# Optimization experiments

Measured on AMD Instinct MI355X. Metric: run time of the kernel, lower is better.

The kernel has to match this reference:

```python
import jax, jax.numpy as jnp
import numpy as np

H = 2048        # hidden_size
NH = 32         # num_heads
HD = H // NH    # head_dim = 64
S = 512         # seq_len
UP = 2          # upsample_ratio
SU = S * UP     # upsampled seq len = 1024
INTER = 5632    # GatedMLP intermediate: int(2048*4*2/3) rounded up to mult of 256
EPS = 1e-6
DEPTH = 1


def rmsnorm(x, w):
    var = jnp.mean(jnp.square(x), axis=-1, keepdims=True)
    return x * jax.lax.rsqrt(var + EPS) * w


def setup_inputs() -> dict:
    key = jax.random.key(0)
    ks = jax.random.split(key, 12)
    sc = 0.02
    return {
        "hidden_states": jax.random.normal(ks[0], (2, S, H), dtype=jnp.float32),
        "W_up": jax.random.normal(ks[1], (SU, S), dtype=jnp.float32) * sc,
        "b_up": jnp.zeros((SU,), dtype=jnp.float32),
        "attn_norm_w": jnp.ones((H,), dtype=jnp.float32),
        "Wq": jax.random.normal(ks[2], (H, H), dtype=jnp.float32) * sc,
        "Wk": jax.random.normal(ks[3], (H, H), dtype=jnp.float32) * sc,
        "Wv": jax.random.normal(ks[4], (H, H), dtype=jnp.float32) * sc,
        "Wo": jax.random.normal(ks[5], (H, H), dtype=jnp.float32) * sc,
        "mlp_norm_w": jnp.ones((H,), dtype=jnp.float32),
        "Wg": jax.random.normal(ks[6], (INTER, H), dtype=jnp.float32) * sc,
        "Wu": jax.random.normal(ks[7], (INTER, H), dtype=jnp.float32) * sc,
        "Wd": jax.random.normal(ks[8], (H, INTER), dtype=jnp.float32) * sc,
    }


def reference(hidden_states, W_up, b_up, attn_norm_w, Wq, Wk, Wv, Wo,
              mlp_norm_w, Wg, Wu, Wd):
    B = hidden_states.shape[0]
    # init_upsampled_tokens: Linear over the sequence axis
    # up[b,t,d] = sum_s h[b,s,d] * W_up[t,s] + b_up[t]
    up = jnp.einsum('bsd,ts->btd', hidden_states, W_up) + b_up[None, :, None]

    for _ in range(DEPTH):
        residual = jnp.concatenate([hidden_states, up], axis=-2)  # [B, S+SU, H]
        x = rmsnorm(up, attn_norm_w)                               # [B, SU, H]
        q = (x @ Wq.T).reshape(B, SU, NH, HD)
        k = (residual @ Wk.T).reshape(B, S + SU, NH, HD)
        v = (residual @ Wv.T).reshape(B, S + SU, NH, HD)
        # explicit (non-causal) cross-attention, full score matrix
        scores = jnp.einsum('bshd,bthd->bsht', q, k) / np.sqrt(HD).astype(np.float32)
        attn = jax.nn.softmax(scores, axis=-1)
        o = jnp.einsum('bsht,bthd->bshd', attn, v).reshape(B, SU, H)
        x = (o @ Wo.T) + x                 # residual onto the *normed* tokens
        x = rmsnorm(x, mlp_norm_w)
        mlp_out = (jax.nn.silu(x @ Wg.T) * (x @ Wu.T)) @ Wd.T
        up = mlp_out + x
    return up
```

## Files before the change

kernel.cpp:

```cpp
#include <hip/hip_runtime.h>

typedef __bf16 bf16;
typedef __bf16 bf16x8 __attribute__((ext_vector_type(8)));
typedef float  f32x4  __attribute__((ext_vector_type(4)));
typedef unsigned int u32x4 __attribute__((ext_vector_type(4)));

#define NB 2
#define SS 512
#define HH 2048
#define SUx 1024
#define TT 1536
#define INTERx 5632

__device__ __forceinline__ void gload16(const void* g, void* l)
{
    __builtin_amdgcn_global_load_lds(
        (const __attribute__((address_space(1))) void*)g,
        (__attribute__((address_space(3))) void*)l, 16, 0, 0);
}

__global__ __launch_bounds__(256)
void cast_k(const float* __restrict__ in, bf16* __restrict__ out, long n)
{
    long i = ((long)blockIdx.x * 256 + threadIdx.x) * 8;
    if (i >= n) return;
    f32x4 a = *(const f32x4*)(in + i);
    f32x4 b = *(const f32x4*)(in + i + 4);
    bf16x8 o;
    o[0]=(bf16)a[0]; o[1]=(bf16)a[1]; o[2]=(bf16)a[2]; o[3]=(bf16)a[3];
    o[4]=(bf16)b[0]; o[5]=(bf16)b[1]; o[6]=(bf16)b[2]; o[7]=(bf16)b[3];
    *(bf16x8*)(out + i) = o;
}

template <typename TIN>
__global__ __launch_bounds__(256)
void transpose_k(const TIN* __restrict__ in, bf16* __restrict__ out,
                 int inRS, int outRS, int nz2,
                 long inZ1, long inZ2, long outZ1, long outZ2)
{
    __shared__ bf16 tile[64][65];
    int z1 = blockIdx.z / nz2, z2 = blockIdx.z % nz2;
    const TIN* ip = in + (long)z1*inZ1 + (long)z2*inZ2
                  + (long)blockIdx.x*64*inRS + (long)blockIdx.y*64;
    bf16* op = out + (long)z1*outZ1 + (long)z2*outZ2
             + (long)blockIdx.y*64*outRS + (long)blockIdx.x*64;
    int tc = threadIdx.x & 63, tr = threadIdx.x >> 6;
    #pragma unroll
    for (int rr = 0; rr < 64; rr += 4)
        tile[rr+tr][tc] = (bf16)(float)ip[(long)(rr+tr)*inRS + tc];
    __syncthreads();
    #pragma unroll
    for (int cc = 0; cc < 64; cc += 4)
        op[(long)(cc+tr)*outRS + tc] = tile[tc][cc+tr];
}

__global__ __launch_bounds__(256)
void rmsnorm_k(const float* __restrict__ x, const float* __restrict__ w,
               bf16* __restrict__ yb, float* __restrict__ yf)
{
    long row = blockIdx.x;
    const float* xp = x + row * HH;
    int t = threadIdx.x;
    f32x4 v0 = *(const f32x4*)(xp + t*8);
    f32x4 v1 = *(const f32x4*)(xp + t*8 + 4);
    float ss = 0.f;
    #pragma unroll
    for (int j = 0; j < 4; ++j) ss += v0[j]*v0[j] + v1[j]*v1[j];
    #pragma unroll
    for (int off = 32; off > 0; off >>= 1) ss += __shfl_xor(ss, off);
    __shared__ float red[4];
    if ((t & 63) == 0) red[t >> 6] = ss;
    __syncthreads();
    float tot = red[0] + red[1] + red[2] + red[3];
    float inv = rsqrtf(tot * (1.0f/(float)HH) + 1e-6f);
    f32x4 w0 = *(const f32x4*)(w + t*8);
    f32x4 w1 = *(const f32x4*)(w + t*8 + 4);
    f32x4 y0, y1; bf16x8 ob;
    #pragma unroll
    for (int j = 0; j < 4; ++j) {
        y0[j] = v0[j] * inv * w0[j];
        y1[j] = v1[j] * inv * w1[j];
        ob[j]   = (bf16)y0[j];
        ob[4+j] = (bf16)y1[j];
    }
    *(bf16x8*)(yb + row*HH + t*8) = ob;
    if (yf) {
        *(f32x4*)(yf + row*HH + t*8)     = y0;
        *(f32x4*)(yf + row*HH + t*8 + 4) = y1;
    }
}

template <int GU>
__global__ __launch_bounds__(512)
void gemm_k(const bf16* __restrict__ A, const bf16* __restrict__ Bw,
            int Nsplit, int K,
            long sA, long sB,
            bf16* __restrict__ Cb, bf16* __restrict__ Cb2, long sCb,
            float* __restrict__ C32, long sC32,
            const float* __restrict__ res, long sRes,
            const float* __restrict__ bias,
            float scale, int doSilu)
{
    __shared__ alignas(16) bf16 As[2][128 * 64];
    __shared__ alignas(16) bf16 Bs[2][128 * 64];
    int z = blockIdx.z;
    const bf16* Ap = A + (long)z * sA;

    int gx = gridDim.x;
    int nwg = gx * gridDim.y;
    int lin = blockIdx.y * gx + blockIdx.x;
    int qq = nwg >> 3, r8 = nwg & 7;
    int xcd = lin & 7, off = lin >> 3;
    int wg = (xcd < r8 ? xcd * (qq + 1) : r8 * (qq + 1) + (xcd - r8) * qq) + off;
    int n0 = (wg % gx) * 128, m0 = (wg / gx) * 128;

    int t = threadIdx.x, lane = t & 63, w = t >> 6;
    int wr = w >> 2, wc = w & 3;
    int lc = lane & 15, lg = lane >> 4;

    int lr = lane >> 3, ls = lane & 7;
    const bf16* gA[2]; const bf16* gB[2];
    int ldsOff[2];
    #pragma unroll
    for (int i = 0; i < 2; ++i) {
        int r = (i*8 + w)*8 + lr;
        gA[i] = Ap + (long)(m0 + r) * K + (ls ^ lr) * 8;
        if (GU) {
            long grow = (long)(n0 >> 1) + (r >> 1);
            gB[i] = Bw + ((r & 1) ? (long)INTERx * K : 0) + grow * K + (ls ^ lr) * 8;
        } else {
            const bf16* Bp = Bw + (long)z * sB;
            gB[i] = Bp + (long)(n0 + r) * K + (ls ^ lr) * 8;
        }
        ldsOff[i] = (i*8 + w) * 512;
    }

    f32x4 zero = {0.f, 0.f, 0.f, 0.f};
    f32x4 acc[4][2];
    #pragma unroll
    for (int i = 0; i < 4; ++i)
        #pragma unroll
        for (int j = 0; j < 2; ++j) acc[i][j] = zero;

    int NKI = K >> 6;
    #pragma unroll
    for (int i = 0; i < 2; ++i) {
        gload16(gA[i], &As[0][0] + ldsOff[i]);
        gload16(gB[i], &Bs[0][0] + ldsOff[i]);
    }
    if (NKI > 1) {
        #pragma unroll
        for (int i = 0; i < 2; ++i) {
            gload16(gA[i] + 64, &As[1][0] + ldsOff[i]);
            gload16(gB[i] + 64, &Bs[1][0] + ldsOff[i]);
        }
    }

    for (int ks = 0; ks < NKI; ++ks) {
        int cur = ks & 1;
        const bf16* Asc = &As[cur][0];
        const bf16* Bsc = &Bs[cur][0];

        if (ks == NKI - 1) asm volatile("s_waitcnt vmcnt(0)" ::: "memory");
        else               asm volatile("s_waitcnt vmcnt(4)" ::: "memory");
        __builtin_amdgcn_s_barrier();
        __builtin_amdgcn_sched_barrier(0);

        #pragma unroll
        for (int kk = 0; kk < 2; ++kk) {
            bf16x8 af[4], bfv[2];
            #pragma unroll
            for (int i = 0; i < 4; ++i) {
                int rA = wr*64 + i*16 + lc;
                af[i]  = *(const bf16x8*)(Asc + rA*64 + (((kk*4 + lg) ^ (rA & 7)) * 8));
            }
            #pragma unroll
            for (int j = 0; j < 2; ++j) {
                int rB = wc*32 + j*16 + lc;
                bfv[j] = *(const bf16x8*)(Bsc + rB*64 + (((kk*4 + lg) ^ (rB & 7)) * 8));
            }
            __builtin_amdgcn_s_setprio(1);
            #pragma unroll
            for (int i = 0; i < 4; ++i)
                #pragma unroll
                for (int j = 0; j < 2; ++j)
                    acc[i][j] = __builtin_amdgcn_mfma_f32_16x16x32_bf16(af[i], bfv[j], acc[i][j], 0, 0, 0);
            __builtin_amdgcn_s_setprio(0);
        }

        __builtin_amdgcn_s_barrier();
        if (ks + 2 < NKI) {
            long ko = (long)(ks + 2) * 64;
            #pragma unroll
            for (int i = 0; i < 2; ++i) {
                gload16(gA[i] + ko, (bf16*)Asc + ldsOff[i]);
                gload16(gB[i] + ko, (bf16*)Bsc + ldsOff[i]);
            }
        }
    }

    if (GU) {
        #pragma unroll
        for (int i = 0; i < 4; ++i) {
            #pragma unroll
            for (int j = 0; j < 2; ++j) {
                int tc2 = wc*32 + j*16 + lc;
                int colp = (n0 >> 1) + (tc2 >> 1);
                #pragma unroll
                for (int r = 0; r < 4; ++r) {
                    int row = m0 + wr*64 + i*16 + lg*4 + r;
                    float v = acc[i][j][r];
                    float pv = __shfl_xor(v, 1);
                    float g  = (lc & 1) ? pv : v;
                    float uu = (lc & 1) ? v  : pv;
                    float prod = (g / (1.f + __expf(-g))) * uu;
                    if (!(lc & 1))
                        Cb[(long)row * Nsplit + colp] = (bf16)prod;
                }
            }
        }
    } else {
        #pragma unroll
        for (int i = 0; i < 4; ++i) {
            #pragma unroll
            for (int j = 0; j < 2; ++j) {
                int col = n0 + wc*32 + j*16 + lc;
                bf16* dst = Cb; int c2 = col;
                if (Cb2 && col >= Nsplit) { dst = Cb2; c2 = col - Nsplit; }
                int firstHalf = (col < Nsplit);
                #pragma unroll
                for (int r = 0; r < 4; ++r) {
                    int row = m0 + wr*64 + i*16 + lg*4 + r;
                    float v = acc[i][j][r] * scale;
                    if (bias)   v += bias[row];
                    if (doSilu && firstHalf) v = v / (1.f + __expf(-v));
                    long off = (long)row * Nsplit + c2;
                    if (res)  v += res[(long)z * sRes + off];
                    if (C32)  C32[(long)z * sC32 + off] = v;
                    if (dst)  dst[(long)z * sCb + off] = (bf16)v;
                }
            }
        }
    }
}

__global__ __launch_bounds__(512)
void attn_k(const bf16* __restrict__ q, const bf16* __restrict__ k,
            const bf16* __restrict__ vt, bf16* __restrict__ o)
{
    int qc = blockIdx.x, h = blockIdx.y, b = blockIdx.z;
    int t = threadIdx.x, lane = t & 63, w = t >> 6;
    int lc = lane & 15, lg = lane >> 4;
    const bf16* qp = q  + ((long)(b*SUx + qc*256 + w*32)) * HH + h*64;
    const bf16* kp = k  + ((long)b*TT) * HH + h*64;
    const bf16* vp = vt + ((long)(b*32 + h)) * 64 * TT;

    __shared__ alignas(16) bf16 Ks[2][64*64];
    __shared__ alignas(16) bf16 Vs[2][64*64];
    __shared__ alignas(16) bf16 Ps[8][2][16*72];

    bf16x8 qf[2][2];
    #pragma unroll
    for (int s = 0; s < 2; ++s)
        #pragma unroll
        for (int kk = 0; kk < 2; ++kk)
            qf[s][kk] = *(const bf16x8*)(qp + (long)(s*16 + lc)*HH + kk*32 + lg*8);

    int lr = lane >> 3, ls = lane & 7;
    int srow = w*8 + lr;
    int sslot = ls ^ lr;
    const bf16* gK = kp + (long)srow * HH + sslot*8;
    const bf16* gV = vp + (long)srow * TT + sslot*8;
    int ldsO = w * 512;

    f32x4 zero = {0.f, 0.f, 0.f, 0.f};
    f32x4 oacc[2][4];
    float lsum[2][4];
    #pragma unroll
    for (int qs = 0; qs < 2; ++qs) {
        #pragma unroll
        for (int r = 0; r < 4; ++r) lsum[qs][r] = 0.f;
        #pragma unroll
        for (int dt = 0; dt < 4; ++dt) oacc[qs][dt] = zero;
    }

    const int NS = TT / 64;
    gload16(gK,            &Ks[0][0] + ldsO);
    gload16(gV,            &Vs[0][0] + ldsO);
    gload16(gK + 64L*HH,   &Ks[1][0] + ldsO);
    gload16(gV + 64,       &Vs[1][0] + ldsO);

    for (int st = 0; st < NS; ++st) {
        int cur = st & 1;
        const bf16* Kc = &Ks[cur][0];
        const bf16* Vc = &Vs[cur][0];

        if (st == NS - 1) asm volatile("s_waitcnt vmcnt(0)" ::: "memory");
        else              asm volatile("s_waitcnt vmcnt(2)" ::: "memory");
        __builtin_amdgcn_s_barrier();
        __builtin_amdgcn_sched_barrier(0);

        bf16x8 kf[4][2];
        #pragma unroll
        for (int s2 = 0; s2 < 4; ++s2) {
            int row = s2*16 + lc;
            #pragma unroll
            for (int kk = 0; kk < 2; ++kk)
                kf[s2][kk] = *(const bf16x8*)(Kc + row*64 + (((kk*4 + lg) ^ (row & 7)) * 8));
        }
        f32x4 sv[2][4];
        __builtin_amdgcn_s_setprio(1);
        #pragma unroll
        for (int qs = 0; qs < 2; ++qs)
            #pragma unroll
            for (int s2 = 0; s2 < 4; ++s2) {
                f32x4 a0 = __builtin_amdgcn_mfma_f32_16x16x32_bf16(qf[qs][0], kf[s2][0], zero, 0, 0, 0);
                sv[qs][s2] = __builtin_amdgcn_mfma_f32_16x16x32_bf16(qf[qs][1], kf[s2][1], a0, 0, 0, 0);
            }
        __builtin_amdgcn_s_setprio(0);

        bf16* Pw = &Ps[w][0][0];
        #pragma unroll
        for (int qs = 0; qs < 2; ++qs)
            #pragma unroll
            for (int r = 0; r < 4; ++r) {
                int prow = lg*4 + r;
                #pragma unroll
                for (int s2 = 0; s2 < 4; ++s2) {
                    float p = __expf(sv[qs][s2][r]);
                    lsum[qs][r] += p;
                    Pw[qs*(16*72) + prow*72 + s2*16 + lc] = (bf16)p;
                }
            }
        asm volatile("s_waitcnt lgkmcnt(0)" ::: "memory");
        __builtin_amdgcn_sched_barrier(0);

        bf16x8 pf[2][2];
        #pragma unroll
        for (int qs = 0; qs < 2; ++qs)
            #pragma unroll
            for (int ks = 0; ks < 2; ++ks)
                pf[qs][ks] = *(const bf16x8*)(Pw + qs*(16*72) + lc*72 + (ks*4 + lg)*8);
        bf16x8 vf[4][2];
        #pragma unroll
        for (int dt = 0; dt < 4; ++dt) {
            int row = dt*16 + lc;
            #pragma unroll
            for (int ks = 0; ks < 2; ++ks)
                vf[dt][ks] = *(const bf16x8*)(Vc + row*64 + (((ks*4 + lg) ^ (row & 7)) * 8));
        }
        __builtin_amdgcn_s_setprio(1);
        #pragma unroll
        for (int qs = 0; qs < 2; ++qs)
            #pragma unroll
            for (int dt = 0; dt < 4; ++dt) {
                oacc[qs][dt] = __builtin_amdgcn_mfma_f32_16x16x32_bf16(pf[qs][0], vf[dt][0], oacc[qs][dt], 0, 0, 0);
                oacc[qs][dt] = __builtin_amdgcn_mfma_f32_16x16x32_bf16(pf[qs][1], vf[dt][1], oacc[qs][dt], 0, 0, 0);
            }
        __builtin_amdgcn_s_setprio(0);

        __builtin_amdgcn_s_barrier();
        if (st + 2 < NS) {
            long t2 = (long)(st + 2) * 64;
            gload16(gK + t2*HH, (bf16*)Kc + ldsO);
            gload16(gV + t2,    (bf16*)Vc + ldsO);
        }
    }

    #pragma unroll
    for (int qs = 0; qs < 2; ++qs)
        #pragma unroll
        for (int r = 0; r < 4; ++r) {
            float l = lsum[qs][r];
            l += __shfl_xor(l, 1);
            l += __shfl_xor(l, 2);
            l += __shfl_xor(l, 4);
            l += __shfl_xor(l, 8);
            float inv = 1.0f / l;
            long row = (long)b*SUx + qc*256 + w*32 + qs*16 + lg*4 + r;
            #pragma unroll
            for (int dt = 0; dt < 4; ++dt)
                o[row*HH + h*64 + dt*16 + lc] = (bf16)(oacc[qs][dt][r] * inv);
        }
}

extern "C" void kernel_launch(void* const* d_in, const int* in_sizes, int n_in,
                              void* d_out, int out_size, void* d_ws, size_t ws_size,
                              hipStream_t stream)
{
    const float* hs  = (const float*)d_in[0];
    const float* Wup = (const float*)d_in[1];
    const float* bup = (const float*)d_in[2];
    const float* anw = (const float*)d_in[3];
    const float* Wq  = (const float*)d_in[4];
    const float* Wk  = (const float*)d_in[5];
    const float* Wv  = (const float*)d_in[6];
    const float* Wo  = (const float*)d_in[7];
    const float* mnw = (const float*)d_in[8];
    const float* Wg  = (const float*)d_in[9];
    const float* Wu  = (const float*)d_in[10];
    const float* Wd  = (const float*)d_in[11];
    float* outp = (float*)d_out;

    char* p = (char*)d_ws;
    auto take = [&](size_t bytes) -> void* {
        void* r = (void*)p;
        p += (bytes + 255) & ~(size_t)255;
        return r;
    };

    bf16* wq  = (bf16*)take((size_t)HH*HH*2);
    bf16* wk  = (bf16*)take(2 * (size_t)HH*HH*2);
    bf16* wv  = wk + (size_t)HH*HH;
    bf16* wo  = (bf16*)take((size_t)HH*HH*2);
    bf16* wgu = (bf16*)take(2 * (size_t)INTERx*HH*2);
    bf16* wd  = (bf16*)take((size_t)INTERx*HH*2);
    bf16* wup = (bf16*)take((size_t)SUx*SS*2);
    bf16* ht  = (bf16*)take((size_t)NB*HH*SS*2);
    bf16* resb= (bf16*)take((size_t)NB*TT*HH*2);
    float* x1f= (float*)take((size_t)NB*SUx*HH*4);
    bf16* x1b = (bf16*)take((size_t)NB*SUx*HH*2);
    float* upf= (float*)take((size_t)NB*SUx*HH*4);

    size_t attn_bytes = (size_t)NB*SUx*HH*2 + 3*(size_t)NB*TT*HH*2 + (size_t)NB*SUx*HH*2;
    size_t mlp_bytes  = (size_t)NB*SUx*HH*4 + (size_t)NB*SUx*HH*2 + (size_t)NB*SUx*INTERx*2;
    char* un = (char*)take(attn_bytes > mlp_bytes ? attn_bytes : mlp_bytes);
    bf16* qb  = (bf16*)un;
    bf16* kb  = qb  + (size_t)NB*SUx*HH;
    bf16* vb  = kb  + (size_t)NB*TT*HH;
    bf16* vtb = vb  + (size_t)NB*TT*HH;
    bf16* ob  = vtb + (size_t)NB*TT*HH;
    float* x2f= (float*)un;
    bf16* x2b = (bf16*)(un + (size_t)NB*SUx*HH*4);
    bf16* gb  = x2b + (size_t)NB*SUx*HH;

    cast_k<<<dim3((unsigned)((size_t)HH*HH/2048)), 256, 0, stream>>>(Wq, wq, (long)HH*HH);
    cast_k<<<dim3((unsigned)((size_t)HH*HH/2048)), 256, 0, stream>>>(Wk, wk, (long)HH*HH);
    cast_k<<<dim3((unsigned)((size_t)HH*HH/2048)), 256, 0, stream>>>(Wv, wv, (long)HH*HH);
    cast_k<<<dim3((unsigned)((size_t)HH*HH/2048)), 256, 0, stream>>>(Wo, wo, (long)HH*HH);
    cast_k<<<dim3((unsigned)((size_t)INTERx*HH/2048)), 256, 0, stream>>>(Wg, wgu, (long)INTERx*HH);
    cast_k<<<dim3((unsigned)((size_t)INTERx*HH/2048)), 256, 0, stream>>>(Wu, wgu + (size_t)INTERx*HH, (long)INTERx*HH);
    cast_k<<<dim3((unsigned)((size_t)INTERx*HH/2048)), 256, 0, stream>>>(Wd, wd, (long)INTERx*HH);
    cast_k<<<dim3((unsigned)((size_t)SUx*SS/2048)), 256, 0, stream>>>(Wup, wup, (long)SUx*SS);
    for (int b = 0; b < NB; ++b)
        cast_k<<<dim3((unsigned)((size_t)SS*HH/2048)), 256, 0, stream>>>(
            hs + (size_t)b*SS*HH, resb + (size_t)b*TT*HH, (long)SS*HH);

    transpose_k<float><<<dim3(SS/64, HH/64, NB), 256, 0, stream>>>(
        hs, ht, HH, SS, 1, (long)SS*HH, 0, (long)HH*SS, 0);

    gemm_k<0><<<dim3(HH/128, SUx/128, NB), 512, 0, stream>>>(
        wup, ht, HH, SS, 0, (long)HH*SS,
        resb + (size_t)SS*HH, nullptr, (long)TT*HH,
        upf, (long)SUx*HH,
        nullptr, 0, bup, 1.0f, 0);

    rmsnorm_k<<<dim3(NB*SUx), 256, 0, stream>>>(upf, anw, x1b, x1f);

    gemm_k<0><<<dim3(HH/128, (NB*SUx)/128, 1), 512, 0, stream>>>(
        x1b, wq, HH, HH, 0, 0, qb, nullptr, 0, nullptr, 0, nullptr, 0, nullptr, 0.125f, 0);
    gemm_k<0><<<dim3((2*HH)/128, (NB*TT)/128, 1), 512, 0, stream>>>(
        resb, wk, HH, HH, 0, 0, kb, vb, 0, nullptr, 0, nullptr, 0, nullptr, 1.0f, 0);

    transpose_k<bf16><<<dim3(TT/64, 1, NB*32), 256, 0, stream>>>(
        vb, vtb, HH, TT, 32, (long)TT*HH, 64, (long)32*64*TT, (long)64*TT);

    attn_k<<<dim3(SUx/256, 32, NB), 512, 0, stream>>>(qb, kb, vtb, ob);

    gemm_k<0><<<dim3(HH/128, (NB*SUx)/128, 1), 512, 0, stream>>>(
        ob, wo, HH, HH, 0, 0, nullptr, nullptr, 0, upf, 0, x1f, 0, nullptr, 1.0f, 0);

    rmsnorm_k<<<dim3(NB*SUx), 256, 0, stream>>>(upf, mnw, x2b, x2f);

    gemm_k<1><<<dim3((2*INTERx)/128, (NB*SUx)/128, 1), 512, 0, stream>>>(
        x2b, wgu, INTERx, HH, 0, 0, gb, nullptr, 0, nullptr, 0, nullptr, 0, nullptr, 1.0f, 0);

    gemm_k<0><<<dim3(HH/128, (NB*SUx)/128, 1), 512, 0, stream>>>(
        gb, wd, HH, INTERx, 0, 0, nullptr, nullptr, 0, outp, 0, x2f, 0, nullptr, 1.0f, 0);

    (void)in_sizes; (void)n_in; (void)out_size; (void)ws_size;
}
```

Before: 535.9 us.

## Add 256x256-tile GEMM with XCD-aware remap and fused SwiGLU for gate/up

Adds a new 256x256-tile bf16 MFMA GEMM kernel with double-buffered direct-to-LDS loads, XOR-swizzled LDS, XCD-aware workgroup remapping and setprio around MFMA phases. It is used only for the MLP gate/up projection. Gate and up weight rows are interleaved in the tile so silu(g)*u can be computed in the epilogue with a lane shuffle, writing only the product. Larger tiles raise arithmetic intensity and cut global traffic, but use 128KB of LDS and more registers, which lowers occupancy, and the grid shrinks to 44x8 workgroups.

```diff
diff --git a/kernel.cpp b/kernel.cpp
--- a/kernel.cpp
+++ b/kernel.cpp
@@ -238,6 +238,148 @@
                     if (res)  v += res[(long)z * sRes + off];
                     if (C32)  C32[(long)z * sC32 + off] = v;
                     if (dst)  dst[(long)z * sCb + off] = (bf16)v;
+                }
+            }
+        }
+    }
+}
+
+template <int GU>
+__global__ __launch_bounds__(512)
+void gemm256_k(const bf16* __restrict__ A, const bf16* __restrict__ Bw,
+               int Nsplit, int K,
+               bf16* __restrict__ Cb, bf16* __restrict__ Cb2)
+{
+    __shared__ alignas(16) bf16 As[2][256 * 64];
+    __shared__ alignas(16) bf16 Bs[2][256 * 64];
+
+    int gx = gridDim.x;
+    int nwg = gx * gridDim.y;
+    int lin = blockIdx.y * gx + blockIdx.x;
+    int qq = nwg >> 3, r8 = nwg & 7;
+    int xcd = lin & 7, off = lin >> 3;
+    int wg = (xcd < r8 ? xcd * (qq + 1) : r8 * (qq + 1) + (xcd - r8) * qq) + off;
+    int n0 = (wg % gx) * 256, m0 = (wg / gx) * 256;
+
+    int t = threadIdx.x, lane = t & 63, w = t >> 6;
+    int wr = w >> 2, wc = w & 3;
+    int lc = lane & 15, lg = lane >> 4;
+
+    int sr = t >> 3, ss_ = t & 7;
+    const bf16* gA[4]; const bf16* gB[4];
+    int ldsO[4];
+    #pragma unroll
+    for (int i = 0; i < 4; ++i) {
+        int r = i*64 + sr;
+        gA[i] = A + (long)(m0 + r) * K + (ss_ ^ (r & 7)) * 8;
+        if (GU) {
+            long grow = (long)(n0 >> 1) + (r >> 1);
+            gB[i] = Bw + ((r & 1) ? (long)INTERx * K : 0) + grow * K + (ss_ ^ (r & 7)) * 8;
+        } else {
+            gB[i] = Bw + (long)(n0 + r) * K + (ss_ ^ (r & 7)) * 8;
+        }
+        ldsO[i] = i * 4096 + t * 8;
+    }
+
+    f32x4 zero = {0.f, 0.f, 0.f, 0.f};
+    f32x4 acc[8][4];
+    #pragma unroll
+    for (int i = 0; i < 8; ++i)
+        #pragma unroll
+        for (int j = 0; j < 4; ++j) acc[i][j] = zero;
+
+    auto stage = [&](int buf, int ti) {
+        long ko = (long)ti * 64;
+        #pragma unroll
+        for (int i = 0; i < 4; ++i)
+            gload16(gA[i] + ko, &As[buf][0] + ldsO[i]);
+        #pragma unroll
+        for (int i = 0; i < 4; ++i)
+            gload16(gB[i] + ko, &Bs[buf][0] + ldsO[i]);
+    };
+
+    int NKI = K >> 6;
+    stage(0, 0);
+    if (NKI > 1) stage(1, 1);
+
+    for (int ks = 0; ks < NKI; ++ks) {
+        int cur = ks & 1;
+        const bf16* Asc = &As[cur][0];
+        const bf16* Bsc = &Bs[cur][0];
+
+        if (ks == NKI - 1) asm volatile("s_waitcnt vmcnt(0)" ::: "memory");
+        else               asm volatile("s_waitcnt vmcnt(8)" ::: "memory");
+        __builtin_amdgcn_s_barrier();
+        __builtin_amdgcn_sched_barrier(0);
+
+        #pragma unroll
+        for (int ph = 0; ph < 4; ++ph) {
+            int mh = ph >> 1, nh = ph & 1;
+            bf16x8 af[4][2], bfv[2][2];
+            #pragma unroll
+            for (int kk = 0; kk < 2; ++kk) {
+                #pragma unroll
+                for (int i = 0; i < 4; ++i) {
+                    int rA = wr*128 + mh*64 + i*16 + lc;
+                    af[i][kk] = *(const bf16x8*)(Asc + (long)rA*64 + (((kk*4 + lg) ^ (rA & 7)) * 8));
+                }
+                #pragma unroll
+                for (int j = 0; j < 2; ++j) {
+                    int rB = wc*64 + nh*32 + j*16 + lc;
+                    bfv[j][kk] = *(const bf16x8*)(Bsc + (long)rB*64 + (((kk*4 + lg) ^ (rB & 7)) * 8));
+                }
+            }
+            asm volatile("s_waitcnt lgkmcnt(0)" ::: "memory");
+            __builtin_amdgcn_sched_barrier(0);
+            __builtin_amdgcn_s_setprio(1);
+            #pragma unroll
+            for (int kk = 0; kk < 2; ++kk)
+                #pragma unroll
+                for (int i = 0; i < 4; ++i)
+                    #pragma unroll
+                    for (int j = 0; j < 2; ++j)
+                        acc[mh*4 + i][nh*2 + j] =
+                            __builtin_amdgcn_mfma_f32_16x16x32_bf16(af[i][kk], bfv[j][kk],
+                                                                    acc[mh*4 + i][nh*2 + j], 0, 0, 0);
+            __builtin_amdgcn_s_setprio(0);
+            __builtin_amdgcn_s_barrier();
+        }
+
+        if (ks + 2 < NKI) stage(cur, ks + 2);
+    }
+
+    if (GU) {
+        #pragma unroll
+        for (int i = 0; i < 8; ++i) {
+            #pragma unroll
+            for (int j = 0; j < 4; ++j) {
+                int tc2 = wc*64 + (j >> 1)*32 + (j & 1)*16 + lc;
+                int colp = (n0 >> 1) + (tc2 >> 1);
+                #pragma unroll
+                for (int r = 0; r < 4; ++r) {
+                    int row = m0 + wr*128 + (i >> 2)*64 + (i & 3)*16 + lg*4 + r;
+                    float v = acc[(i >> 2)*4 + (i & 3)][j][r];
+                    float pv = __shfl_xor(v, 1);
+                    float g  = (lc & 1) ? pv : v;
+                    float uu = (lc & 1) ? v  : pv;
+                    float prod = (g / (1.f + __expf(-g))) * uu;
+                    if (!(lc & 1))
+                        Cb[(long)row * Nsplit + colp] = (bf16)prod;
+                }
+            }
+        }
+    } else {
+        #pragma unroll
+        for (int i = 0; i < 8; ++i) {
+            #pragma unroll
+            for (int j = 0; j < 4; ++j) {
+                int col = n0 + wc*64 + (j >> 1)*32 + (j & 1)*16 + lc;
+                bf16* dst = Cb; int c2 = col;
+                if (Cb2 && col >= Nsplit) { dst = Cb2; c2 = col - Nsplit; }
+                #pragma unroll
+                for (int r = 0; r < 4; ++r) {
+                    int row = m0 + wr*128 + (i >> 2)*64 + (i & 3)*16 + lg*4 + r;
+                    dst[(long)row * Nsplit + c2] = (bf16)acc[i][j][r];
                 }
             }
         }
@@ -472,8 +614,8 @@
 
     rmsnorm_k<<<dim3(NB*SUx), 256, 0, stream>>>(upf, mnw, x2b, x2f);
 
-    gemm_k<1><<<dim3((2*INTERx)/128, (NB*SUx)/128, 1), 512, 0, stream>>>(
-        x2b, wgu, INTERx, HH, 0, 0, gb, nullptr, 0, nullptr, 0, nullptr, 0, nullptr, 1.0f, 0);
+    gemm256_k<1><<<dim3((2*INTERx)/256, (NB*SUx)/256, 1), 512, 0, stream>>>(
+        x2b, wgu, INTERx, HH, gb, nullptr);
 
     gemm_k<0><<<dim3(HH/128, (NB*SUx)/128, 1), 512, 0, stream>>>(
         gb, wd, HH, INTERx, 0, 0, nullptr, nullptr, 0, outp, 0, x2f, 0, nullptr, 1.0f, 0);
```

Result: slower. 592.8 us (+10.6%).
